# Kernel tuning notes

Measured on AMD Instinct MI355X. Metric: run time of the kernel, lower is better.

## Reference

```python
import jax, jax.numpy as jnp
import numpy as np

HIDDEN = 1024
HEADS = 16
HEAD_DIM = HIDDEN // HEADS


def setup_inputs() -> dict:
    key = jax.random.key(0)
    ks = jax.random.split(key, 9)
    s = 1.0 / np.sqrt(HIDDEN)
    x = jax.random.normal(ks[0], (1, 4096, HIDDEN), dtype=jnp.float32)
    return {
        "x": x,
        "wq": jax.random.normal(ks[1], (HIDDEN, HIDDEN), dtype=jnp.float32) * s,
        "bq": jnp.zeros((HIDDEN,), dtype=jnp.float32),
        "wk": jax.random.normal(ks[2], (HIDDEN, HIDDEN), dtype=jnp.float32) * s,
        "bk": jnp.zeros((HIDDEN,), dtype=jnp.float32),
        "wv": jax.random.normal(ks[3], (HIDDEN, HIDDEN), dtype=jnp.float32) * s,
        "bv": jnp.zeros((HIDDEN,), dtype=jnp.float32),
        "wo": jax.random.normal(ks[4], (HIDDEN, HIDDEN), dtype=jnp.float32) * s,
        "bo": jnp.zeros((HIDDEN,), dtype=jnp.float32),
    }


def reference(x, wq, bq, wk, bk, wv, bv, wo, bo):
    B, S, D = x.shape
    H, Hd = HEADS, HEAD_DIM
    # projections (torch Linear: y = x @ W.T + b)
    q = (x @ wq.T + bq).reshape(B, S, H, Hd).transpose(0, 2, 1, 3)  # [B,H,S,Hd]
    k = (x @ wk.T + bk).reshape(B, S, H, Hd).transpose(0, 2, 1, 3)
    v = (x @ wv.T + bv).reshape(B, S, H, Hd).transpose(0, 2, 1, 3)
    scores = jnp.einsum("bhqd,bhkd->bhqk", q, k) / jnp.sqrt(jnp.float32(Hd))
    attn = jax.nn.softmax(scores, axis=-1)  # full [B,H,S,S] matrix, faithful to source
    out = jnp.einsum("bhqk,bhkd->bhqd", attn, v)  # [B,H,S,Hd]
    out = out.transpose(0, 2, 1, 3).reshape(B, S, D)
    return out @ wo.T + bo
```

## Files before the change

kernel.cpp:

```cpp
#include <hip/hip_runtime.h>
#include <stdint.h>

#define S 4096
#define D 1024
#define H 16
#define HD 64

#define QK_SCALE 0.18033688011112042f

typedef short short8  __attribute__((ext_vector_type(8)));
typedef float floatx4 __attribute__((ext_vector_type(4)));
typedef float floatx16 __attribute__((ext_vector_type(16)));

__device__ __forceinline__ unsigned short f2bf(float f) {
  union { float f; unsigned int i; } x; x.f = f;
  unsigned int r = x.i + 0x7FFFu + ((x.i >> 16) & 1u);
  return (unsigned short)(r >> 16);
}

#if defined(__has_builtin)
#if __has_builtin(__builtin_amdgcn_cvt_pk_bf16_f32)
#define HAVE_PK_BF16 1
#endif
#endif
__device__ __forceinline__ unsigned int pkbf(float a, float b) {
#ifdef HAVE_PK_BF16
  typedef __bf16 bf2_t __attribute__((ext_vector_type(2)));
  bf2_t t = __builtin_amdgcn_cvt_pk_bf16_f32(a, b);
  return __builtin_bit_cast(unsigned int, t);
#else
  return (unsigned int)f2bf(a) | ((unsigned int)f2bf(b) << 16);
#endif
}

__global__ __launch_bounds__(256) void cvt_kernel(
    const float* __restrict__ x,  unsigned short* __restrict__ xb,
    const float* __restrict__ wq, unsigned short* __restrict__ wqb,
    const float* __restrict__ wk, unsigned short* __restrict__ wkb,
    const float* __restrict__ wv, unsigned short* __restrict__ wvb,
    const float* __restrict__ wo, unsigned short* __restrict__ wob,
    const float* __restrict__ bq, float* __restrict__ bqs)
{
  const int z = blockIdx.y;
  const float* s; unsigned short* d;
  float scale = 1.f;
  if (z < 4)       { s = x + (size_t)z * 1048576; d = xb + (size_t)z * 1048576; }
  else if (z == 4) { s = wq; d = wqb; scale = QK_SCALE; }
  else if (z == 5) { s = wk; d = wkb; }
  else if (z == 6) { s = wv; d = wvb; }
  else             { s = wo; d = wob; }
  const size_t i = ((size_t)blockIdx.x * 256 + threadIdx.x) * 4;
  float4 v = *reinterpret_cast<const float4*>(s + i);
  uint2 o;
  o.x = pkbf(v.x * scale, v.y * scale);
  o.y = pkbf(v.z * scale, v.w * scale);
  *reinterpret_cast<uint2*>(d + i) = o;
  if (z == 4 && blockIdx.x == 0) {
    const int t = threadIdx.x;
    #pragma unroll
    for (int j = 0; j < 4; ++j) bqs[t * 4 + j] = bq[t * 4 + j] * QK_SCALE;
  }
}

__global__ __launch_bounds__(256) void gemm_bt(
    const unsigned short* __restrict__ X,
    const unsigned short* __restrict__ W0, const float* __restrict__ B0, unsigned short* __restrict__ C0,
    const unsigned short* __restrict__ W1, const float* __restrict__ B1, unsigned short* __restrict__ C1,
    const unsigned short* __restrict__ W2, const float* __restrict__ B2, unsigned short* __restrict__ C2,
    float* __restrict__ Cf, unsigned short* __restrict__ VtOut)
{
  const unsigned short* W; const float* Bb; unsigned short* C;
  const int z = blockIdx.z;
  if (z == 0)      { W = W0; Bb = B0; C = C0; }
  else if (z == 1) { W = W1; Bb = B1; C = C1; }
  else             { W = W2; Bb = B2; C = C2; }

  const int bm = blockIdx.y, bn = blockIdx.x;
  const int tid  = threadIdx.x;
  const int lane = tid & 63, wave = tid >> 6;
  const int quad = lane >> 4, n16 = lane & 15;
  const int wm = (wave >> 1) * 64, wn = (wave & 1) * 64;

  __shared__ unsigned short As[128 * 40];
  __shared__ unsigned short Bs[128 * 40];
  __shared__ unsigned short Ts[64 * 136];

  floatx4 zero = {0.f, 0.f, 0.f, 0.f};
  floatx4 acc[4][4];
  #pragma unroll
  for (int i = 0; i < 4; ++i)
    #pragma unroll
    for (int j = 0; j < 4; ++j) acc[i][j] = zero;

  const int r1 = tid >> 2, kc = (tid & 3) * 8;
  const unsigned short* Xa = X + (size_t)(bm * 128 + r1) * D + kc;
  const unsigned short* Wa = W + (size_t)(bn * 128 + r1) * D + kc;

  for (int k0 = 0; k0 < D; k0 += 32) {
    __syncthreads();
    uint4 a0 = *reinterpret_cast<const uint4*>(Xa + k0);
    uint4 a1 = *reinterpret_cast<const uint4*>(Xa + (size_t)64 * D + k0);
    uint4 b0 = *reinterpret_cast<const uint4*>(Wa + k0);
    uint4 b1 = *reinterpret_cast<const uint4*>(Wa + (size_t)64 * D + k0);
    *reinterpret_cast<uint4*>(&As[r1 * 40 + kc])        = a0;
    *reinterpret_cast<uint4*>(&As[(r1 + 64) * 40 + kc]) = a1;
    *reinterpret_cast<uint4*>(&Bs[r1 * 40 + kc])        = b0;
    *reinterpret_cast<uint4*>(&Bs[(r1 + 64) * 40 + kc]) = b1;
    __syncthreads();

    short8 af[4], bfr[4];
    #pragma unroll
    for (int t = 0; t < 4; ++t) {
      af[t]  = *reinterpret_cast<const short8*>(&As[(wm + t * 16 + n16) * 40 + quad * 8]);
      bfr[t] = *reinterpret_cast<const short8*>(&Bs[(wn + t * 16 + n16) * 40 + quad * 8]);
    }
    #pragma unroll
    for (int tm = 0; tm < 4; ++tm)
      #pragma unroll
      for (int tn = 0; tn < 4; ++tn)
        acc[tm][tn] = __builtin_amdgcn_mfma_f32_16x16x32_bf16(af[tm], bfr[tn], acc[tm][tn], 0, 0, 0);
  }

  if (z == 2 && VtOut) {
    #pragma unroll
    for (int p = 0; p < 2; ++p) {
      __syncthreads();
      if ((wn >> 6) == p) {
        #pragma unroll
        for (int tn = 0; tn < 4; ++tn) {
          const int col = bn * 128 + p * 64 + tn * 16 + n16;
          const float bias = Bb[col];
          #pragma unroll
          for (int tm = 0; tm < 4; ++tm) {
            uint2 w;
            w.x = pkbf(acc[tm][tn][0] + bias, acc[tm][tn][1] + bias);
            w.y = pkbf(acc[tm][tn][2] + bias, acc[tm][tn][3] + bias);
            *reinterpret_cast<uint2*>(&Ts[(tn * 16 + n16) * 136 + wm + tm * 16 + quad * 4]) = w;
          }
        }
      }
      __syncthreads();
      {
        const int rl = tid >> 2, cc = (tid & 3) * 32;
        uint4 t0 = *reinterpret_cast<const uint4*>(&Ts[rl * 136 + cc]);
        uint4 t1 = *reinterpret_cast<const uint4*>(&Ts[rl * 136 + cc + 8]);
        uint4 t2 = *reinterpret_cast<const uint4*>(&Ts[rl * 136 + cc + 16]);
        uint4 t3 = *reinterpret_cast<const uint4*>(&Ts[rl * 136 + cc + 24]);
        const size_t go = (size_t)(bn * 128 + p * 64 + rl) * S + bm * 128 + cc;
        *reinterpret_cast<uint4*>(&VtOut[go])      = t0;
        *reinterpret_cast<uint4*>(&VtOut[go + 8])  = t1;
        *reinterpret_cast<uint4*>(&VtOut[go + 16]) = t2;
        *reinterpret_cast<uint4*>(&VtOut[go + 24]) = t3;
      }
    }
    return;
  }

  #pragma unroll
  for (int tn = 0; tn < 4; ++tn) {
    const int col = bn * 128 + wn + tn * 16 + n16;
    const float bias = Bb[col];
    #pragma unroll
    for (int tm = 0; tm < 4; ++tm) {
      const int rowb = bm * 128 + wm + tm * 16 + quad * 4;
      #pragma unroll
      for (int r = 0; r < 4; ++r) {
        const float v = acc[tm][tn][r] + bias;
        if (Cf) Cf[(size_t)(rowb + r) * D + col] = v;
        else    C[(size_t)(rowb + r) * D + col]  = f2bf(v);
      }
    }
  }
}

__global__ __launch_bounds__(256, 4) void attn(
    const unsigned short* __restrict__ Q,
    const unsigned short* __restrict__ K,
    const unsigned short* __restrict__ Vt,
    unsigned short* __restrict__ Op,
    float* __restrict__ Ls)
{
  const int h   = blockIdx.y;
  const int z   = blockIdx.z;
  const int q0  = blockIdx.x * 128;
  const int key0 = z * (S / 2);
  const int tid = threadIdx.x;
  const int lane = tid & 63, wave = tid >> 6;
  const int l31 = lane & 31, h8 = lane >> 5;

  __shared__ unsigned short Ks[64 * 72];
  __shared__ unsigned short Vs[64 * 72];
  __shared__ unsigned short Pq[4][32 * 72];

  const int qrow = q0 + wave * 32 + l31;
  short8 qf[4];
  #pragma unroll
  for (int ks = 0; ks < 4; ++ks)
    qf[ks] = *reinterpret_cast<const short8*>(Q + (size_t)qrow * D + h * HD + ks * 16 + h8 * 8);

  floatx16 o0 = {}, o1 = {};
  float lsum = 0.f;

  const int r1 = tid >> 2, c16 = (tid & 3) * 16;
  const unsigned short* Kbase = K  + (size_t)(key0 + r1) * D + h * HD + c16;
  const unsigned short* Vbase = Vt + (size_t)(h * HD + r1) * S + key0 + c16;

  uint4 ka, kb, va, vb;
  ka = *reinterpret_cast<const uint4*>(Kbase);
  kb = *reinterpret_cast<const uint4*>(Kbase + 8);
  va = *reinterpret_cast<const uint4*>(Vbase);
  vb = *reinterpret_cast<const uint4*>(Vbase + 8);

  const int NIT = (S / 2) / 64;
  for (int kt = 0; kt < NIT; ++kt) {
    __syncthreads();
    *reinterpret_cast<uint4*>(&Ks[r1 * 72 + c16])     = ka;
    *reinterpret_cast<uint4*>(&Ks[r1 * 72 + c16 + 8]) = kb;
    *reinterpret_cast<uint4*>(&Vs[r1 * 72 + c16])     = va;
    *reinterpret_cast<uint4*>(&Vs[r1 * 72 + c16 + 8]) = vb;
    __syncthreads();

    const int kn = (kt < NIT - 1) ? kt + 1 : kt;
    ka = *reinterpret_cast<const uint4*>(Kbase + (size_t)kn * 64 * D);
    kb = *reinterpret_cast<const uint4*>(Kbase + (size_t)kn * 64 * D + 8);
    va = *reinterpret_cast<const uint4*>(Vbase + kn * 64);
    vb = *reinterpret_cast<const uint4*>(Vbase + kn * 64 + 8);

    floatx16 s0 = {}, s1 = {};
    #pragma unroll
    for (int ks = 0; ks < 4; ++ks) {
      short8 a0 = *reinterpret_cast<const short8*>(&Ks[l31 * 72 + ks * 16 + h8 * 8]);
      short8 a1 = *reinterpret_cast<const short8*>(&Ks[(32 + l31) * 72 + ks * 16 + h8 * 8]);
      s0 = __builtin_amdgcn_mfma_f32_32x32x16_bf16(a0, qf[ks], s0, 0, 0, 0);
      s1 = __builtin_amdgcn_mfma_f32_32x32x16_bf16(a1, qf[ks], s1, 0, 0, 0);
    }

    float rs = 0.f;
    #pragma unroll
    for (int r = 0; r < 16; ++r) {
      s0[r] = exp2f(s0[r]); rs += s0[r];
      s1[r] = exp2f(s1[r]); rs += s1[r];
    }
    rs += __shfl_xor(rs, 32);
    lsum += rs;

    unsigned short* pw = &Pq[wave][l31 * 72];
    #pragma unroll
    for (int rg = 0; rg < 4; ++rg) {
      uint2 w0, w1;
      w0.x = pkbf(s0[rg * 4 + 0], s0[rg * 4 + 1]);
      w0.y = pkbf(s0[rg * 4 + 2], s0[rg * 4 + 3]);
      w1.x = pkbf(s1[rg * 4 + 0], s1[rg * 4 + 1]);
      w1.y = pkbf(s1[rg * 4 + 2], s1[rg * 4 + 3]);
      *reinterpret_cast<uint2*>(&pw[rg * 8 + h8 * 4])      = w0;
      *reinterpret_cast<uint2*>(&pw[32 + rg * 8 + h8 * 4]) = w1;
    }

    short8 pb[4];
    #pragma unroll
    for (int ks = 0; ks < 4; ++ks)
      pb[ks] = *reinterpret_cast<const short8*>(&Pq[wave][l31 * 72 + ks * 16 + h8 * 8]);
    #pragma unroll
    for (int ks = 0; ks < 4; ++ks) {
      short8 va0 = *reinterpret_cast<const short8*>(&Vs[l31 * 72 + ks * 16 + h8 * 8]);
      short8 va1 = *reinterpret_cast<const short8*>(&Vs[(32 + l31) * 72 + ks * 16 + h8 * 8]);
      o0 = __builtin_amdgcn_mfma_f32_32x32x16_bf16(va0, pb[ks], o0, 0, 0, 0);
      o1 = __builtin_amdgcn_mfma_f32_32x32x16_bf16(va1, pb[ks], o1, 0, 0, 0);
    }
  }

  if (h8 == 0) Ls[(size_t)z * S * H + qrow * H + h] = lsum;

  unsigned short* ob = Op + (size_t)z * S * D + (size_t)qrow * D + h * HD;
  #pragma unroll
  for (int rg = 0; rg < 4; ++rg) {
    uint2 w0, w1;
    w0.x = pkbf(o0[rg * 4 + 0], o0[rg * 4 + 1]);
    w0.y = pkbf(o0[rg * 4 + 2], o0[rg * 4 + 3]);
    w1.x = pkbf(o1[rg * 4 + 0], o1[rg * 4 + 1]);
    w1.y = pkbf(o1[rg * 4 + 2], o1[rg * 4 + 3]);
    *reinterpret_cast<uint2*>(&ob[rg * 8 + h8 * 4])      = w0;
    *reinterpret_cast<uint2*>(&ob[32 + rg * 8 + h8 * 4]) = w1;
  }
}

__global__ __launch_bounds__(256) void combine(
    unsigned short* __restrict__ Op,
    const float* __restrict__ Ls)
{
  const size_t e8 = ((size_t)blockIdx.x * 256 + threadIdx.x) * 8;
  const int q = (int)(e8 >> 10);
  const int col = (int)(e8 & 1023);
  const int hh = col >> 6;
  const float l = Ls[q * H + hh] + Ls[S * H + q * H + hh];
  const float inv = 1.f / l;
  uint4 a = *reinterpret_cast<const uint4*>(Op + e8);
  uint4 b = *reinterpret_cast<const uint4*>(Op + (size_t)S * D + e8);
  uint4 r;
  const unsigned int* au = &a.x; const unsigned int* bu = &b.x; unsigned int* ru = &r.x;
  #pragma unroll
  for (int w = 0; w < 4; ++w) {
    union { unsigned int i; float f; } alo, ahi, blo, bhi;
    alo.i = au[w] << 16;          ahi.i = au[w] & 0xFFFF0000u;
    blo.i = bu[w] << 16;          bhi.i = bu[w] & 0xFFFF0000u;
    ru[w] = pkbf((alo.f + blo.f) * inv, (ahi.f + bhi.f) * inv);
  }
  *reinterpret_cast<uint4*>(Op + e8) = r;
}

extern "C" void kernel_launch(void* const* d_in, const int* in_sizes, int n_in,
                              void* d_out, int out_size, void* d_ws, size_t ws_size,
                              hipStream_t stream) {
  const float* x  = (const float*)d_in[0];
  const float* wq = (const float*)d_in[1];
  const float* bq = (const float*)d_in[2];
  const float* wk = (const float*)d_in[3];
  const float* bk = (const float*)d_in[4];
  const float* wv = (const float*)d_in[5];
  const float* bv = (const float*)d_in[6];
  const float* wo = (const float*)d_in[7];
  const float* bo = (const float*)d_in[8];
  float* out = (float*)d_out;

  unsigned short* ws = (unsigned short*)d_ws;
  const size_t SD = (size_t)S * D;
  const size_t DD = (size_t)D * D;
  unsigned short* xb  = ws;
  unsigned short* wqb = xb + SD;
  unsigned short* wkb = wqb + DD;
  unsigned short* wvb = wkb + DD;
  unsigned short* wob = wvb + DD;
  unsigned short* Qw  = wob + DD;
  unsigned short* Kw  = Qw + SD;
  unsigned short* Vtw = Kw + SD;
  unsigned short* Op  = Vtw + SD;
  float* Ls  = (float*)(Op + 2 * SD);
  float* bqs = Ls + 2 * (size_t)S * H;

  dim3 blk(256);
  cvt_kernel<<<dim3(1024, 8), blk, 0, stream>>>(x, xb, wq, wqb, wk, wkb, wv, wvb, wo, wob, bq, bqs);
  gemm_bt<<<dim3(D / 128, S / 128, 3), blk, 0, stream>>>(
      xb, wqb, bqs, Qw, wkb, bk, Kw, wvb, bv, nullptr, nullptr, Vtw);
  attn<<<dim3(S / 128, H, 2), blk, 0, stream>>>(Qw, Kw, Vtw, Op, Ls);
  combine<<<dim3(SD / (256 * 8)), blk, 0, stream>>>(Op, Ls);
  gemm_bt<<<dim3(D / 128, S / 128, 1), blk, 0, stream>>>(
      Op, wob, bo, nullptr, wob, bo, nullptr, wob, bo, nullptr, out, nullptr);
}
```

Baseline: 292.8 us.

## Process 64 query rows per wave in attention and use raw exp2

Each wave in the attention kernel now handles two 32-row query groups instead of one. Each loaded K and V tile in shared memory is reused across twice as many queries, which halves the tile loads and barriers per query, and the grid shrinks to half as many blocks. The softmax exponent now calls the raw hardware exp2 builtin when it is available, avoiding the range-handling wrapper. The costs are about twice the accumulator registers, a larger per-wave P buffer in LDS, and launch bounds lowered to 2 blocks per CU, so occupancy drops and the smaller grid of 512 blocks may fill the GPU less evenly.

```diff
diff --git a/kernel.cpp b/kernel.cpp
--- a/kernel.cpp
+++ b/kernel.cpp
@@ -22,7 +22,11 @@
 #if __has_builtin(__builtin_amdgcn_cvt_pk_bf16_f32)
 #define HAVE_PK_BF16 1
 #endif
-#endif
+#if __has_builtin(__builtin_amdgcn_exp2f)
+#define HAVE_RAW_EXP2 1
+#endif
+#endif
+
 __device__ __forceinline__ unsigned int pkbf(float a, float b) {
 #ifdef HAVE_PK_BF16
   typedef __bf16 bf2_t __attribute__((ext_vector_type(2)));
@@ -30,6 +34,14 @@
   return __builtin_bit_cast(unsigned int, t);
 #else
   return (unsigned int)f2bf(a) | ((unsigned int)f2bf(b) << 16);
+#endif
+}
+
+__device__ __forceinline__ float fexp2(float x) {
+#ifdef HAVE_RAW_EXP2
+  return __builtin_amdgcn_exp2f(x);
+#else
+  return exp2f(x);
 #endif
 }
 
@@ -173,33 +185,36 @@
   }
 }
 
-__global__ __launch_bounds__(256, 4) void attn(
+__global__ __launch_bounds__(256, 2) void attn(
     const unsigned short* __restrict__ Q,
     const unsigned short* __restrict__ K,
     const unsigned short* __restrict__ Vt,
     unsigned short* __restrict__ Op,
     float* __restrict__ Ls)
 {
-  const int h   = blockIdx.y;
-  const int z   = blockIdx.z;
-  const int q0  = blockIdx.x * 128;
+  const int h    = blockIdx.y;
+  const int z    = blockIdx.z;
+  const int q0   = blockIdx.x * 256;
   const int key0 = z * (S / 2);
-  const int tid = threadIdx.x;
+  const int tid  = threadIdx.x;
   const int lane = tid & 63, wave = tid >> 6;
   const int l31 = lane & 31, h8 = lane >> 5;
 
   __shared__ unsigned short Ks[64 * 72];
   __shared__ unsigned short Vs[64 * 72];
-  __shared__ unsigned short Pq[4][32 * 72];
-
-  const int qrow = q0 + wave * 32 + l31;
-  short8 qf[4];
-  #pragma unroll
-  for (int ks = 0; ks < 4; ++ks)
-    qf[ks] = *reinterpret_cast<const short8*>(Q + (size_t)qrow * D + h * HD + ks * 16 + h8 * 8);
-
-  floatx16 o0 = {}, o1 = {};
-  float lsum = 0.f;
+  __shared__ unsigned short Pq[4][64 * 72];
+
+  const int qA = q0 + wave * 64 + l31;
+  const int qB = qA + 32;
+  short8 qfA[4], qfB[4];
+  #pragma unroll
+  for (int ks = 0; ks < 4; ++ks) {
+    qfA[ks] = *reinterpret_cast<const short8*>(Q + (size_t)qA * D + h * HD + ks * 16 + h8 * 8);
+    qfB[ks] = *reinterpret_cast<const short8*>(Q + (size_t)qB * D + h * HD + ks * 16 + h8 * 8);
+  }
+
+  floatx16 oA0 = {}, oA1 = {}, oB0 = {}, oB1 = {};
+  float lsumA = 0.f, lsumB = 0.f;
 
   const int r1 = tid >> 2, c16 = (tid & 3) * 16;
   const unsigned short* Kbase = K  + (size_t)(key0 + r1) * D + h * HD + c16;
@@ -226,61 +241,90 @@
     va = *reinterpret_cast<const uint4*>(Vbase + kn * 64);
     vb = *reinterpret_cast<const uint4*>(Vbase + kn * 64 + 8);
 
-    floatx16 s0 = {}, s1 = {};
+    floatx16 sA0 = {}, sA1 = {}, sB0 = {}, sB1 = {};
     #pragma unroll
     for (int ks = 0; ks < 4; ++ks) {
       short8 a0 = *reinterpret_cast<const short8*>(&Ks[l31 * 72 + ks * 16 + h8 * 8]);
       short8 a1 = *reinterpret_cast<const short8*>(&Ks[(32 + l31) * 72 + ks * 16 + h8 * 8]);
-      s0 = __builtin_amdgcn_mfma_f32_32x32x16_bf16(a0, qf[ks], s0, 0, 0, 0);
-      s1 = __builtin_amdgcn_mfma_f32_32x32x16_bf16(a1, qf[ks], s1, 0, 0, 0);
-    }
-
-    float rs = 0.f;
+      sA0 = __builtin_amdgcn_mfma_f32_32x32x16_bf16(a0, qfA[ks], sA0, 0, 0, 0);
+      sA1 = __builtin_amdgcn_mfma_f32_32x32x16_bf16(a1, qfA[ks], sA1, 0, 0, 0);
+      sB0 = __builtin_amdgcn_mfma_f32_32x32x16_bf16(a0, qfB[ks], sB0, 0, 0, 0);
+      sB1 = __builtin_amdgcn_mfma_f32_32x32x16_bf16(a1, qfB[ks], sB1, 0, 0, 0);
+    }
+
+    float rsA = 0.f, rsB = 0.f;
     #pragma unroll
     for (int r = 0; r < 16; ++r) {
-      s0[r] = exp2f(s0[r]); rs += s0[r];
-      s1[r] = exp2f(s1[r]); rs += s1[r];
-    }
-    rs += __shfl_xor(rs, 32);
-    lsum += rs;
-
-    unsigned short* pw = &Pq[wave][l31 * 72];
+      sA0[r] = fexp2(sA0[r]); rsA += sA0[r];
+      sA1[r] = fexp2(sA1[r]); rsA += sA1[r];
+      sB0[r] = fexp2(sB0[r]); rsB += sB0[r];
+      sB1[r] = fexp2(sB1[r]); rsB += sB1[r];
+    }
+    rsA += __shfl_xor(rsA, 32);
+    rsB += __shfl_xor(rsB, 32);
+    lsumA += rsA;
+    lsumB += rsB;
+
+    unsigned short* pwA = &Pq[wave][l31 * 72];
+    unsigned short* pwB = &Pq[wave][(32 + l31) * 72];
     #pragma unroll
     for (int rg = 0; rg < 4; ++rg) {
       uint2 w0, w1;
-      w0.x = pkbf(s0[rg * 4 + 0], s0[rg * 4 + 1]);
-      w0.y = pkbf(s0[rg * 4 + 2], s0[rg * 4 + 3]);
-      w1.x = pkbf(s1[rg * 4 + 0], s1[rg * 4 + 1]);
-      w1.y = pkbf(s1[rg * 4 + 2], s1[rg * 4 + 3]);
-      *reinterpret_cast<uint2*>(&pw[rg * 8 + h8 * 4])      = w0;
-      *reinterpret_cast<uint2*>(&pw[32 + rg * 8 + h8 * 4]) = w1;
-    }
-
-    short8 pb[4];
-    #pragma unroll
-    for (int ks = 0; ks < 4; ++ks)
-      pb[ks] = *reinterpret_cast<const short8*>(&Pq[wave][l31 * 72 + ks * 16 + h8 * 8]);
+      w0.x = pkbf(sA0[rg * 4 + 0], sA0[rg * 4 + 1]);
+      w0.y = pkbf(sA0[rg * 4 + 2], sA0[rg * 4 + 3]);
+      w1.x = pkbf(sA1[rg * 4 + 0], sA1[rg * 4 + 1]);
+      w1.y = pkbf(sA1[rg * 4 + 2], sA1[rg * 4 + 3]);
+      *reinterpret_cast<uint2*>(&pwA[rg * 8 + h8 * 4])      = w0;
+      *reinterpret_cast<uint2*>(&pwA[32 + rg * 8 + h8 * 4]) = w1;
+      uint2 v0, v1;
+      v0.x = pkbf(sB0[rg * 4 + 0], sB0[rg * 4 + 1]);
+      v0.y = pkbf(sB0[rg * 4 + 2], sB0[rg * 4 + 3]);
+      v1.x = pkbf(sB1[rg * 4 + 0], sB1[rg * 4 + 1]);
+      v1.y = pkbf(sB1[rg * 4 + 2], sB1[rg * 4 + 3]);
+      *reinterpret_cast<uint2*>(&pwB[rg * 8 + h8 * 4])      = v0;
+      *reinterpret_cast<uint2*>(&pwB[32 + rg * 8 + h8 * 4]) = v1;
+    }
+
+    short8 pbA[4], pbB[4];
+    #pragma unroll
+    for (int ks = 0; ks < 4; ++ks) {
+      pbA[ks] = *reinterpret_cast<const short8*>(&Pq[wave][l31 * 72 + ks * 16 + h8 * 8]);
+      pbB[ks] = *reinterpret_cast<const short8*>(&Pq[wave][(32 + l31) * 72 + ks * 16 + h8 * 8]);
+    }
     #pragma unroll
     for (int ks = 0; ks < 4; ++ks) {
       short8 va0 = *reinterpret_cast<const short8*>(&Vs[l31 * 72 + ks * 16 + h8 * 8]);
       short8 va1 = *reinterpret_cast<const short8*>(&Vs[(32 + l31) * 72 + ks * 16 + h8 * 8]);
-      o0 = __builtin_amdgcn_mfma_f32_32x32x16_bf16(va0, pb[ks], o0, 0, 0, 0);
-      o1 = __builtin_amdgcn_mfma_f32_32x32x16_bf16(va1, pb[ks], o1, 0, 0, 0);
-    }
-  }
-
-  if (h8 == 0) Ls[(size_t)z * S * H + qrow * H + h] = lsum;
-
-  unsigned short* ob = Op + (size_t)z * S * D + (size_t)qrow * D + h * HD;
+      oA0 = __builtin_amdgcn_mfma_f32_32x32x16_bf16(va0, pbA[ks], oA0, 0, 0, 0);
+      oA1 = __builtin_amdgcn_mfma_f32_32x32x16_bf16(va1, pbA[ks], oA1, 0, 0, 0);
+      oB0 = __builtin_amdgcn_mfma_f32_32x32x16_bf16(va0, pbB[ks], oB0, 0, 0, 0);
+      oB1 = __builtin_amdgcn_mfma_f32_32x32x16_bf16(va1, pbB[ks], oB1, 0, 0, 0);
+    }
+  }
+
+  if (h8 == 0) {
+    Ls[(size_t)z * S * H + qA * H + h] = lsumA;
+    Ls[(size_t)z * S * H + qB * H + h] = lsumB;
+  }
+
+  unsigned short* obA = Op + (size_t)z * S * D + (size_t)qA * D + h * HD;
+  unsigned short* obB = Op + (size_t)z * S * D + (size_t)qB * D + h * HD;
   #pragma unroll
   for (int rg = 0; rg < 4; ++rg) {
     uint2 w0, w1;
-    w0.x = pkbf(o0[rg * 4 + 0], o0[rg * 4 + 1]);
-    w0.y = pkbf(o0[rg * 4 + 2], o0[rg * 4 + 3]);
-    w1.x = pkbf(o1[rg * 4 + 0], o1[rg * 4 + 1]);
-    w1.y = pkbf(o1[rg * 4 + 2], o1[rg * 4 + 3]);
-    *reinterpret_cast<uint2*>(&ob[rg * 8 + h8 * 4])      = w0;
-    *reinterpret_cast<uint2*>(&ob[32 + rg * 8 + h8 * 4]) = w1;
+    w0.x = pkbf(oA0[rg * 4 + 0], oA0[rg * 4 + 1]);
+    w0.y = pkbf(oA0[rg * 4 + 2], oA0[rg * 4 + 3]);
+    w1.x = pkbf(oA1[rg * 4 + 0], oA1[rg * 4 + 1]);
+    w1.y = pkbf(oA1[rg * 4 + 2], oA1[rg * 4 + 3]);
+    *reinterpret_cast<uint2*>(&obA[rg * 8 + h8 * 4])      = w0;
+    *reinterpret_cast<uint2*>(&obA[32 + rg * 8 + h8 * 4]) = w1;
+    uint2 v0, v1;
+    v0.x = pkbf(oB0[rg * 4 + 0], oB0[rg * 4 + 1]);
+    v0.y = pkbf(oB0[rg * 4 + 2], oB0[rg * 4 + 3]);
+    v1.x = pkbf(oB1[rg * 4 + 0], oB1[rg * 4 + 1]);
+    v1.y = pkbf(oB1[rg * 4 + 2], oB1[rg * 4 + 3]);
+    *reinterpret_cast<uint2*>(&obB[rg * 8 + h8 * 4])      = v0;
+    *reinterpret_cast<uint2*>(&obB[32 + rg * 8 + h8 * 4]) = v1;
   }
 }
 
@@ -341,7 +385,7 @@
   cvt_kernel<<<dim3(1024, 8), blk, 0, stream>>>(x, xb, wq, wqb, wk, wkb, wv, wvb, wo, wob, bq, bqs);
   gemm_bt<<<dim3(D / 128, S / 128, 3), blk, 0, stream>>>(
       xb, wqb, bqs, Qw, wkb, bk, Kw, wvb, bv, nullptr, nullptr, Vtw);
-  attn<<<dim3(S / 128, H, 2), blk, 0, stream>>>(Qw, Kw, Vtw, Op, Ls);
+  attn<<<dim3(S / 256, H, 2), blk, 0, stream>>>(Qw, Kw, Vtw, Op, Ls);
   combine<<<dim3(SD / (256 * 8)), blk, 0, stream>>>(Op, Ls);
   gemm_bt<<<dim3(D / 128, S / 128, 1), blk, 0, stream>>>(
       Op, wob, bo, nullptr, wob, bo, nullptr, wob, bo, nullptr, out, nullptr);
```

Result: faster. 265.3 us (-9.4%).
